# Optimization experiments

Hardware: AMD Instinct MI355X
Metric: run time of the kernel (lower is better)

## Reference

```python
import jax, jax.numpy as jnp
import numpy as np

EPS = 1e-6
N_HEADS, N_POINTS = 6, 4


def layer_norm(x, w, b):
    m = jnp.mean(x, -1, keepdims=True)
    v = jnp.mean((x - m) ** 2, -1, keepdims=True)
    return (x - m) * jax.lax.rsqrt(v + EPS) * w + b


def bilinear_sample(val, loc, Hl, Wl):
    # val: (B, nH, Hl*Wl, d); loc: (B, Lq, nH, P, 2) in [0,1]
    # matches F.grid_sample(mode='bilinear', padding='zeros', align_corners=False)
    B, nH, _, d = val.shape
    Lq, P = loc.shape[1], loc.shape[3]
    x = loc[..., 0] * Wl - 0.5
    y = loc[..., 1] * Hl - 0.5
    x0 = jnp.floor(x)
    y0 = jnp.floor(y)
    wx1 = x - x0
    wy1 = y - y0
    out = jnp.zeros((B, nH, Lq * P, d), val.dtype)
    corners = ((0, 0, (1 - wy1) * (1 - wx1)), (0, 1, (1 - wy1) * wx1),
               (1, 0, wy1 * (1 - wx1)), (1, 1, wy1 * wx1))
    for dy, dx, w in corners:
        xi = x0 + dx
        yi = y0 + dy
        valid = (xi >= 0) & (xi < Wl) & (yi >= 0) & (yi < Hl)
        xi_c = jnp.clip(xi, 0, Wl - 1).astype(jnp.int32)
        yi_c = jnp.clip(yi, 0, Hl - 1).astype(jnp.int32)
        idx = (yi_c * Wl + xi_c).transpose(0, 2, 1, 3).reshape(B, nH, Lq * P)
        g = jnp.take_along_axis(val, idx[..., None], axis=2)  # (B,nH,Lq*P,d)
        ww = jnp.where(valid, w, 0.0).transpose(0, 2, 1, 3).reshape(B, nH, Lq * P)
        out = out + g * ww[..., None]
    return out.reshape(B, nH, Lq, P, d).transpose(0, 2, 1, 3, 4)  # (B,Lq,nH,P,d)


def dwconv3x3(x, w, b):
    # x: (N, C, H, W); w: (C, 1, 3, 3) depthwise
    y = jax.lax.conv_general_dilated(x, w, (1, 1), 'SAME',
                                     feature_group_count=w.shape[0],
                                     dimension_numbers=('NCHW', 'OIHW', 'NCHW'))
    return y + b[None, :, None, None]


def setup_inputs() -> dict:
    key = jax.random.key(0)
    ks = jax.random.split(key, 16)
    B, H, W, C = 8, 32, 32, 768
    Lq = 3 * H * W
    Hf = Wf = 64
    hidden = int(C * 0.25)
    s = 0.02
    inp = {
        'query': jax.random.normal(ks[0], (B, Lq, C), jnp.float32),
        'reference_points': jax.random.uniform(ks[1], (B, Lq, 1, 2), jnp.float32),
        'feat': jax.random.normal(ks[2], (B, Hf * Wf, C), jnp.float32),
        'spatial_shapes': jnp.array([[Hf, Wf]], jnp.int32),
        'level_start_index': jnp.zeros((1,), jnp.int32),
        'H': H, 'W': W,
        'qn_w': jnp.ones((C,)), 'qn_b': jnp.zeros((C,)),
        'fn_w': jnp.ones((C,)), 'fn_b': jnp.zeros((C,)),
        'so_w': jax.random.normal(ks[3], (C, N_HEADS * N_POINTS * 2)) * s,
        'so_b': jax.random.normal(ks[4], (N_HEADS * N_POINTS * 2,)) * s,
        'aw_w': jax.random.normal(ks[5], (C, N_HEADS * N_POINTS)) * s,
        'aw_b': jnp.zeros((N_HEADS * N_POINTS,)),
        'vp_w': jax.random.normal(ks[6], (C, C)) * s,
        'vp_b': jnp.zeros((C,)),
        'op_w': jax.random.normal(ks[7], (C, C)) * s,
        'op_b': jnp.zeros((C,)),
        'ffn_w': jnp.ones((C,)), 'ffn_b': jnp.zeros((C,)),
        'fc1_w': jax.random.normal(ks[8], (C, hidden)) * s,
        'fc1_b': jnp.zeros((hidden,)),
        'dw_w': jax.random.normal(ks[9], (hidden, 1, 3, 3)) * s,
        'dw_b': jnp.zeros((hidden,)),
        'fc2_w': jax.random.normal(ks[10], (hidden, C)) * s,
        'fc2_b': jnp.zeros((C,)),
    }
    return inp


def reference(query, reference_points, feat, spatial_shapes, level_start_index, H, W,
              qn_w, qn_b, fn_w, fn_b, so_w, so_b, aw_w, aw_b, vp_w, vp_b, op_w, op_b,
              ffn_w, ffn_b, fc1_w, fc1_b, dw_w, dw_b, fc2_w, fc2_b):
    B, Lq, C = query.shape
    nH, nP = N_HEADS, N_POINTS
    d = C // nH
    ss = np.asarray(spatial_shapes)
    Hl, Wl = int(ss[0, 0]), int(ss[0, 1])

    # --- MSDeformAttn (single level) ---
    q = layer_norm(query, qn_w, qn_b)
    f = layer_norm(feat, fn_w, fn_b)
    value = (f @ vp_w + vp_b).reshape(B, Hl * Wl, nH, d).transpose(0, 2, 1, 3)  # (B,nH,Lin,d)
    offs = (q @ so_w + so_b).reshape(B, Lq, nH, 1, nP, 2)
    aw = jax.nn.softmax((q @ aw_w + aw_b).reshape(B, Lq, nH, nP), axis=-1)
    normalizer = jnp.array([Wl, Hl], query.dtype)
    loc = reference_points[:, :, None, :, None, :] + offs / normalizer  # (B,Lq,nH,1,nP,2)
    sampled = bilinear_sample(value, loc[:, :, :, 0], Hl, Wl)           # (B,Lq,nH,nP,d)
    attn = (sampled * aw[..., None]).sum(3).reshape(B, Lq, C) @ op_w + op_b
    query = query + attn

    # --- ConvFFN (3 equal HxW chunks through shared depthwise conv) ---
    x = layer_norm(query, ffn_w, ffn_b) @ fc1_w + fc1_b  # (B, 3*H*W, hid)
    n = Lq // 3
    hid = fc1_w.shape[1]
    xc = x.reshape(B, 3, n, hid).transpose(0, 1, 3, 2).reshape(B * 3, hid, H, W)
    xc = dwconv3x3(xc, dw_w, dw_b)
    x = xc.reshape(B, 3, hid, n).transpose(0, 1, 3, 2).reshape(B, Lq, hid)
    x = jax.nn.gelu(x, approximate=False)
    x = x @ fc2_w + fc2_b
    return query + x
```

## Files before the change

### kernel.cpp

```cpp
#include <hip/hip_runtime.h>
#include <hip/hip_bf16.h>
#include <math.h>

typedef __hip_bfloat16 bf16;
typedef short bf16x8 __attribute__((ext_vector_type(8)));
typedef float f32x4 __attribute__((ext_vector_type(4)));

#define NB 8
#define LQ 3072
#define CC 768
#define NHEADS 6
#define NPTS 4
#define DHEAD 128
#define HLVL 64
#define WLVL 64
#define LIN 4096
#define HID 192
#define BLTOT 24576
#define FROWS 32768

__global__ __launch_bounds__(256)
void ln_bf16_kernel(const float* __restrict__ x, const float* __restrict__ w,
                    const float* __restrict__ b, bf16* __restrict__ out)
{
    const int row = blockIdx.x;
    const int t = threadIdx.x;
    const float* xr = x + (size_t)row * CC;
    float v0 = xr[t], v1 = xr[t + 256], v2 = xr[t + 512];
    float s = v0 + v1 + v2;
    float ss = v0 * v0 + v1 * v1 + v2 * v2;
    #pragma unroll
    for (int o = 32; o > 0; o >>= 1) {
        s += __shfl_down(s, o);
        ss += __shfl_down(ss, o);
    }
    __shared__ float red[8];
    const int lane = t & 63, wv = t >> 6;
    if (lane == 0) { red[wv] = s; red[4 + wv] = ss; }
    __syncthreads();
    if (t == 0) {
        float S = red[0] + red[1] + red[2] + red[3];
        float SS = red[4] + red[5] + red[6] + red[7];
        float m = S * (1.f / CC);
        float var = SS * (1.f / CC) - m * m;
        red[0] = m; red[1] = rsqrtf(var + 1e-6f);
    }
    __syncthreads();
    const float m = red[0], rs = red[1];
    bf16* o = out + (size_t)row * CC;
    o[t]       = __float2bfloat16((v0 - m) * rs * w[t] + b[t]);
    o[t + 256] = __float2bfloat16((v1 - m) * rs * w[t + 256] + b[t + 256]);
    o[t + 512] = __float2bfloat16((v2 - m) * rs * w[t + 512] + b[t + 512]);
}

__global__ __launch_bounds__(256)
void wt_bf16_kernel(const float* __restrict__ src, bf16* __restrict__ dst, int K, int N)
{
    __shared__ float t[64][65];
    const int tn0 = blockIdx.x * 64, tk0 = blockIdx.y * 64;
    const int r = threadIdx.x >> 6, c = threadIdx.x & 63;
    #pragma unroll
    for (int i = 0; i < 16; ++i) {
        const int k = i * 4 + r;
        t[k][c] = src[(size_t)(tk0 + k) * N + tn0 + c];
    }
    __syncthreads();
    #pragma unroll
    for (int i = 0; i < 16; ++i) {
        const int n = i * 4 + r;
        dst[(size_t)(tn0 + n) * K + tk0 + c] = __float2bfloat16(t[c][n]);
    }
}

__global__ __launch_bounds__(256)
void build_dots_w(const float* __restrict__ so_w, const float* __restrict__ so_b,
                  const float* __restrict__ aw_w, const float* __restrict__ aw_b,
                  bf16* __restrict__ wt, float* __restrict__ db)
{
    int i = blockIdx.x * 256 + threadIdx.x;
    if (i < 128 * 768) {
        int n = i / 768, k = i - n * 768;
        float v = 0.f;
        if (n < 48) v = so_w[(size_t)k * 48 + n];
        else if (n < 72) v = aw_w[(size_t)k * 24 + (n - 48)];
        wt[i] = __float2bfloat16(v);
    }
    if (i < 128) {
        float bv = 0.f;
        if (i < 48) bv = so_b[i];
        else if (i < 72) bv = aw_b[i - 48];
        db[i] = bv;
    }
}

template<int N_>
__device__ __forceinline__ void wait_vmcnt()
{
    if constexpr (N_ == 0)      asm volatile("s_waitcnt vmcnt(0)" ::: "memory");
    else if constexpr (N_ == 4) asm volatile("s_waitcnt vmcnt(4)" ::: "memory");
    else if constexpr (N_ == 6) asm volatile("s_waitcnt vmcnt(6)" ::: "memory");
    else if constexpr (N_ == 8) asm volatile("s_waitcnt vmcnt(8)" ::: "memory");
    else static_assert(N_ == 0 || N_ == 4 || N_ == 6 || N_ == 8, "add a vmcnt case");
}

template<int BM, int BN, int WM, int WN, int MODE>
__global__ __launch_bounds__(256)
void gemm_kernel(const bf16* __restrict__ A, const bf16* __restrict__ Bt,
                 const float* __restrict__ bias, const float* __restrict__ res,
                 void* __restrict__ outv, int M, int N, int K)
{
    constexpr int WAVES_N = BN / WN;
    constexpr int FM = WM / 16, FN = WN / 16;
    constexpr int CWA = BM / 32;
    constexpr int CWB = BN / 32;
    constexpr int LPT = CWA + CWB;
    constexpr int ABYTES = BM * 256;
    constexpr int DBUF_BYTES = (BM + BN) * 256;
    constexpr int EPI_BYTES = BM * BN * 4;
    constexpr size_t SMEM_BYTES = DBUF_BYTES > EPI_BYTES ? DBUF_BYTES : EPI_BYTES;
    __shared__ __align__(16) char smem[SMEM_BYTES];
    bf16* sA = (bf16*)smem;
    bf16* sB = (bf16*)(smem + ABYTES);
    float* epi = (float*)smem;

    const int tid = threadIdx.x;
    const int lane = tid & 63;
    const int wave = tid >> 6;

    const int nwgx = gridDim.x;
    const int nwg = nwgx * gridDim.y;
    const int bid = blockIdx.y * nwgx + blockIdx.x;
    const int swz = (bid & 7) * (nwg >> 3) + (bid >> 3);
    const int m0 = (swz / nwgx) * BM;
    const int n0 = (swz % nwgx) * BN;

    const int wm = (wave / WAVES_N) * WM;
    const int wn = (wave % WAVES_N) * WN;

    const int srow = lane >> 3;
    const int scol = ((lane & 7) ^ srow) * 8;

#define STAGE(tt, half)                                                                            \
    { const int k0_ = (tt) * 64;                                                                   \
      _Pragma("unroll")                                                                            \
      for (int i_ = 0; i_ < CWA; ++i_) {                                                           \
        const int c_ = i_ * 4 + wave;                                                              \
        __builtin_amdgcn_global_load_lds(                                                          \
          (const __attribute__((address_space(1))) void*)(A + (size_t)(m0 + c_ * 8 + srow) * K + k0_ + scol), \
          (__attribute__((address_space(3))) void*)(sA + (half) * (BM * 64) + c_ * 512), 16, 0, 0); } \
      _Pragma("unroll")                                                                            \
      for (int i_ = 0; i_ < CWB; ++i_) {                                                           \
        const int c_ = i_ * 4 + wave;                                                              \
        __builtin_amdgcn_global_load_lds(                                                          \
          (const __attribute__((address_space(1))) void*)(Bt + (size_t)(n0 + c_ * 8 + srow) * K + k0_ + scol), \
          (__attribute__((address_space(3))) void*)(sB + (half) * (BN * 64) + c_ * 512), 16, 0, 0); } }

    f32x4 acc[FM][FN] = {};
    const int nt = K >> 6;

    STAGE(0, 0);
    STAGE(1, 1);

    for (int t = 0; t < nt; ++t) {
        const int half = t & 1;
        if (t + 1 < nt) wait_vmcnt<LPT>();
        else            wait_vmcnt<0>();
        __builtin_amdgcn_s_barrier();
        const bf16* cA = sA + half * (BM * 64);
        const bf16* cB = sB + half * (BN * 64);
        #pragma unroll
        for (int kki = 0; kki < 2; ++kki) {
            const int kslot = kki * 4 + (lane >> 4);
            bf16x8 aF[FM], bF[FN];
            #pragma unroll
            for (int i = 0; i < FM; ++i) {
                const int row = wm + i * 16 + (lane & 15);
                aF[i] = *(const bf16x8*)(&cA[row * 64 + ((kslot ^ (row & 7)) * 8)]);
            }
            #pragma unroll
            for (int j = 0; j < FN; ++j) {
                const int row = wn + j * 16 + (lane & 15);
                bF[j] = *(const bf16x8*)(&cB[row * 64 + ((kslot ^ (row & 7)) * 8)]);
            }
            #pragma unroll
            for (int i = 0; i < FM; ++i) {
                #pragma unroll
                for (int j = 0; j < FN; ++j)
                    acc[i][j] = __builtin_amdgcn_mfma_f32_16x16x32_bf16(aF[i], bF[j], acc[i][j], 0, 0, 0);
            }
        }
        asm volatile("s_waitcnt lgkmcnt(0)" ::: "memory");
        __builtin_amdgcn_s_barrier();
        if (t + 2 < nt) STAGE(t + 2, half);
    }
#undef STAGE

    #pragma unroll
    for (int j = 0; j < FN; ++j) {
        const int colL = wn + j * 16 + (lane & 15);
        const float bj = bias[n0 + colL];
        #pragma unroll
        for (int i = 0; i < FM; ++i) {
            #pragma unroll
            for (int r = 0; r < 4; ++r) {
                const int rowL = wm + i * 16 + ((lane >> 4) << 2) + r;
                const int addr = rowL * BN + ((((colL >> 2) ^ (rowL & 7)) << 2) | (colL & 3));
                epi[addr] = acc[i][j][r] + bj;
            }
        }
    }
    __syncthreads();

    if constexpr (MODE == 0) {
        constexpr int GPR = BN / 8;
        constexpr int GPT = (BM * BN / 8) / 256;
        #pragma unroll
        for (int k = 0; k < GPT; ++k) {
            const int f = k * 256 + tid;
            const int rr = f / GPR, cc = (f % GPR) * 8;
            const int g0 = ((cc >> 2) ^ (rr & 7)) << 2;
            const int g1 = (((cc >> 2) + 1) ^ (rr & 7)) << 2;
            float4 v0 = *(const float4*)&epi[rr * BN + g0];
            float4 v1 = *(const float4*)&epi[rr * BN + g1];
            bf16 tmp[8];
            tmp[0] = __float2bfloat16(v0.x); tmp[1] = __float2bfloat16(v0.y);
            tmp[2] = __float2bfloat16(v0.z); tmp[3] = __float2bfloat16(v0.w);
            tmp[4] = __float2bfloat16(v1.x); tmp[5] = __float2bfloat16(v1.y);
            tmp[6] = __float2bfloat16(v1.z); tmp[7] = __float2bfloat16(v1.w);
            *(bf16x8*)((bf16*)outv + (size_t)(m0 + rr) * N + n0 + cc) = *(bf16x8*)tmp;
        }
    } else {
        constexpr int QPR = BN / 4;
        constexpr int QPT = (BM * BN / 4) / 256;
        #pragma unroll
        for (int k = 0; k < QPT; ++k) {
            const int f = k * 256 + tid;
            const int rr = f / QPR, cc = (f % QPR) * 4;
            const int gs = ((cc >> 2) ^ (rr & 7)) << 2;
            float4 v = *(const float4*)&epi[rr * BN + gs];
            const size_t gidx = (size_t)(m0 + rr) * N + n0 + cc;
            if constexpr (MODE == 1) {
                float4 q = *(const float4*)&res[gidx];
                v.x += q.x; v.y += q.y; v.z += q.z; v.w += q.w;
            }
            *(float4*)&((float*)outv)[gidx] = v;
        }
    }
}

__global__ __launch_bounds__(256)
void locsoftmax_kernel(const float* __restrict__ dots, const float* __restrict__ refp,
                       float4* __restrict__ params)
{
    int i = blockIdx.x * 256 + threadIdx.x;
    if (i >= BLTOT * NHEADS) return;
    int bl = i / NHEADS, h = i - bl * NHEADS;
    const float* d = dots + (size_t)bl * 128;
    float rx = refp[(size_t)bl * 2], ry = refp[(size_t)bl * 2 + 1];
    float l0 = d[48 + h * 4 + 0], l1 = d[48 + h * 4 + 1];
    float l2 = d[48 + h * 4 + 2], l3 = d[48 + h * 4 + 3];
    float mx = fmaxf(fmaxf(l0, l1), fmaxf(l2, l3));
    float e0 = expf(l0 - mx), e1 = expf(l1 - mx), e2 = expf(l2 - mx), e3 = expf(l3 - mx);
    float inv = 1.f / (e0 + e1 + e2 + e3);
    float ee[4] = {e0, e1, e2, e3};
    #pragma unroll
    for (int p = 0; p < 4; ++p) {
        float ox = d[h * 8 + p * 2], oy = d[h * 8 + p * 2 + 1];
        params[(size_t)i * 4 + p] =
            make_float4(rx + ox * (1.f / WLVL), ry + oy * (1.f / HLVL), ee[p] * inv, 0.f);
    }
}

__global__ __launch_bounds__(256)
void sampler_kernel(const bf16* __restrict__ value, const float4* __restrict__ params,
                    bf16* __restrict__ attn_in)
{
    const int tid = threadIdx.x;
    const int g = blockIdx.x * 16 + (tid >> 4);
    const int lane16 = tid & 15;
    const int bl = g / NHEADS;
    const int h = g - bl * NHEADS;
    const int b = bl / LQ;
    const bf16* vh = value + (size_t)b * LIN * CC + h * DHEAD + lane16 * 8;

    int offs[16];
    float wgt[16];
    #pragma unroll
    for (int p = 0; p < NPTS; ++p) {
        float4 pr = params[(size_t)g * 4 + p];
        float x = pr.x * (float)WLVL - 0.5f;
        float y = pr.y * (float)HLVL - 0.5f;
        float x0f = floorf(x), y0f = floorf(y);
        float wx1 = x - x0f, wy1 = y - y0f;
        float wx0 = 1.f - wx1, wy0 = 1.f - wy1;
        int x0 = (int)x0f, y0 = (int)y0f;
        #pragma unroll
        for (int dy = 0; dy < 2; ++dy) {
            const int yi = y0 + dy;
            const int yc = min(max(yi, 0), HLVL - 1);
            const float wy = (dy ? wy1 : wy0) * ((yi >= 0 && yi < HLVL) ? pr.z : 0.f);
            #pragma unroll
            for (int dx = 0; dx < 2; ++dx) {
                const int xi = x0 + dx;
                const int xc = min(max(xi, 0), WLVL - 1);
                const int idx = p * 4 + dy * 2 + dx;
                offs[idx] = (yc * WLVL + xc) * CC;
                wgt[idx] = wy * (dx ? wx1 : wx0) * ((xi >= 0 && xi < WLVL) ? 1.f : 0.f);
            }
        }
    }
    bf16x8 v[16];
    #pragma unroll
    for (int i = 0; i < 16; ++i) v[i] = *(const bf16x8*)(vh + offs[i]);
    float acc[8] = {};
    #pragma unroll
    for (int i = 0; i < 16; ++i) {
        #pragma unroll
        for (int j = 0; j < 8; ++j)
            acc[j] += wgt[i] * __uint_as_float(((unsigned)(unsigned short)v[i][j]) << 16);
    }
    bf16 tmp[8];
    #pragma unroll
    for (int j = 0; j < 8; ++j) tmp[j] = __float2bfloat16(acc[j]);
    *(bf16x8*)(attn_in + (size_t)bl * CC + h * DHEAD + lane16 * 8) = *(bf16x8*)tmp;
}

__global__ void dwconv_gelu_kernel(const float* __restrict__ z, const float* __restrict__ dw_w,
                                   const float* __restrict__ dw_b, bf16* __restrict__ g)
{
    const int m = blockIdx.x;
    const int c = threadIdx.x;
    const int pix = m & 1023;
    const int h = pix >> 5, w = pix & 31;
    float acc = dw_b[c];
    #pragma unroll
    for (int dy = -1; dy <= 1; ++dy) {
        int hh2 = h + dy;
        if (hh2 < 0 || hh2 >= 32) continue;
        #pragma unroll
        for (int dx = -1; dx <= 1; ++dx) {
            int ww2 = w + dx;
            if (ww2 < 0 || ww2 >= 32) continue;
            acc += z[(size_t)(m + dy * 32 + dx) * HID + c] * dw_w[c * 9 + (dy + 1) * 3 + (dx + 1)];
        }
    }
    float ge = acc * 0.5f * (1.f + erff(acc * 0.70710678118f));
    g[(size_t)m * HID + c] = __float2bfloat16(ge);
}

extern "C" void kernel_launch(void* const* d_in, const int* in_sizes, int n_in,
                              void* d_out, int out_size, void* d_ws, size_t ws_size,
                              hipStream_t stream)
{
    const float* query = (const float*)d_in[0];
    const float* refp  = (const float*)d_in[1];
    const float* feat  = (const float*)d_in[2];
    const float* qn_w = (const float*)d_in[7];
    const float* qn_b = (const float*)d_in[8];
    const float* fn_w = (const float*)d_in[9];
    const float* fn_b = (const float*)d_in[10];
    const float* so_w = (const float*)d_in[11];
    const float* so_b = (const float*)d_in[12];
    const float* aw_w = (const float*)d_in[13];
    const float* aw_b = (const float*)d_in[14];
    const float* vp_w = (const float*)d_in[15];
    const float* vp_b = (const float*)d_in[16];
    const float* op_w = (const float*)d_in[17];
    const float* op_b = (const float*)d_in[18];
    const float* ffn_w = (const float*)d_in[19];
    const float* ffn_b = (const float*)d_in[20];
    const float* fc1_w = (const float*)d_in[21];
    const float* fc1_b = (const float*)d_in[22];
    const float* dw_w = (const float*)d_in[23];
    const float* dw_b = (const float*)d_in[24];
    const float* fc2_w = (const float*)d_in[25];
    const float* fc2_b = (const float*)d_in[26];
    float* out = (float*)d_out;

    if (ws_size < (size_t)125829632) return;
    char* ws = (char*)d_ws;
    bf16* vp_wt   = (bf16*)(ws + 0);
    bf16* op_wt   = (bf16*)(ws + 1179648);
    bf16* fc1_wt  = (bf16*)(ws + 2359296);
    bf16* fc2_wt  = (bf16*)(ws + 2654208);
    bf16* dots_wt = (bf16*)(ws + 2949120);
    float* dots_b = (float*)(ws + 3145728);
    float4* params = (float4*)(ws + 3146240);
    float* dots_out = (float*)(ws + 12583424);
    char* regA = ws + 25166336;
    char* regB = ws + 75497984;
    bf16* f_ln    = (bf16*)regA;
    bf16* attn_in = (bf16*)regA;
    float* z      = (float*)regA;
    bf16* q_ln  = (bf16*)regB;
    bf16* value = (bf16*)regB;
    bf16* y     = (bf16*)regB;
    bf16* g     = (bf16*)regB;

    wt_bf16_kernel<<<dim3(12, 12), 256, 0, stream>>>(vp_w, vp_wt, 768, 768);
    wt_bf16_kernel<<<dim3(12, 12), 256, 0, stream>>>(op_w, op_wt, 768, 768);
    wt_bf16_kernel<<<dim3(3, 12), 256, 0, stream>>>(fc1_w, fc1_wt, 768, 192);
    wt_bf16_kernel<<<dim3(12, 3), 256, 0, stream>>>(fc2_w, fc2_wt, 192, 768);
    build_dots_w<<<384, 256, 0, stream>>>(so_w, so_b, aw_w, aw_b, dots_wt, dots_b);

    ln_bf16_kernel<<<BLTOT, 256, 0, stream>>>(query, qn_w, qn_b, q_ln);
    gemm_kernel<64, 128, 32, 64, 2><<<dim3(1, BLTOT / 64), 256, 0, stream>>>(
        q_ln, dots_wt, dots_b, nullptr, dots_out, BLTOT, 128, 768);
    locsoftmax_kernel<<<(BLTOT * NHEADS + 255) / 256, 256, 0, stream>>>(dots_out, refp, params);
    ln_bf16_kernel<<<FROWS, 256, 0, stream>>>(feat, fn_w, fn_b, f_ln);
    gemm_kernel<128, 128, 64, 64, 0><<<dim3(6, FROWS / 128), 256, 0, stream>>>(
        f_ln, vp_wt, vp_b, nullptr, value, FROWS, 768, 768);
    sampler_kernel<<<(BLTOT * NHEADS) / 16, 256, 0, stream>>>(value, params, attn_in);
    gemm_kernel<64, 128, 32, 64, 1><<<dim3(6, BLTOT / 64), 256, 0, stream>>>(
        attn_in, op_wt, op_b, query, out, BLTOT, 768, 768);

    ln_bf16_kernel<<<BLTOT, 256, 0, stream>>>(out, ffn_w, ffn_b, y);
    gemm_kernel<64, 64, 16, 64, 2><<<dim3(3, BLTOT / 64), 256, 0, stream>>>(
        y, fc1_wt, fc1_b, nullptr, z, BLTOT, HID, 768);
    dwconv_gelu_kernel<<<BLTOT, HID, 0, stream>>>(z, dw_w, dw_b, g);
    gemm_kernel<64, 128, 32, 64, 1><<<dim3(6, BLTOT / 64), 256, 0, stream>>>(
        g, fc2_wt, fc2_b, out, out, BLTOT, 768, HID);
}
```

Measured before the change: 347.6 us.

## Store intermediate residual and fc1 output in bf16, prefetch residual, vectorize LN/dwconv

The attention output-projection GEMM now writes the residual sum as bf16 instead of fp32, and the FFN LayerNorm reads that bf16 tensor with a wave-per-row vectorized kernel. fc1 output is stored in bf16, and the depthwise conv + GELU kernel processes four channels per thread with vector loads. The final GEMM adds a bf16 residual that is prefetched into registers before the main loop, and the dots GEMM uses a smaller tile to launch more blocks. This cuts memory traffic across several stages but rounds the residual stream to bf16, which reduces accuracy of the final output.

```diff
diff --git a/kernel.cpp b/kernel.cpp
--- a/kernel.cpp
+++ b/kernel.cpp
@@ -4,6 +4,7 @@
 
 typedef __hip_bfloat16 bf16;
 typedef short bf16x8 __attribute__((ext_vector_type(8)));
+typedef short bf16x4 __attribute__((ext_vector_type(4)));
 typedef float f32x4 __attribute__((ext_vector_type(4)));
 
 #define NB 8
@@ -19,6 +20,9 @@
 #define BLTOT 24576
 #define FROWS 32768
 
+__device__ __forceinline__ float bf2f(short u)
+{ return __uint_as_float(((unsigned)(unsigned short)u) << 16); }
+
 __global__ __launch_bounds__(256)
 void ln_bf16_kernel(const float* __restrict__ x, const float* __restrict__ w,
                     const float* __restrict__ b, bf16* __restrict__ out)
@@ -54,6 +58,48 @@
 }
 
 __global__ __launch_bounds__(256)
+void ln_bf16in_kernel(const bf16* __restrict__ x, const float* __restrict__ w,
+                      const float* __restrict__ b, bf16* __restrict__ out)
+{
+    const int row = blockIdx.x * 4 + (threadIdx.x >> 6);
+    const int lane = threadIdx.x & 63;
+    const bf16* xr = x + (size_t)row * CC;
+    bf16x8 v8 = *(const bf16x8*)(xr + lane * 8);
+    bf16x4 v4 = *(const bf16x4*)(xr + 512 + lane * 4);
+    float v[12];
+    #pragma unroll
+    for (int j = 0; j < 8; ++j) v[j] = bf2f(v8[j]);
+    #pragma unroll
+    for (int j = 0; j < 4; ++j) v[8 + j] = bf2f(v4[j]);
+    float s = 0.f, ss = 0.f;
+    #pragma unroll
+    for (int j = 0; j < 12; ++j) { s += v[j]; ss += v[j] * v[j]; }
+    #pragma unroll
+    for (int o = 32; o > 0; o >>= 1) {
+        s += __shfl_down(s, o);
+        ss += __shfl_down(ss, o);
+    }
+    s = __shfl(s, 0); ss = __shfl(ss, 0);
+    const float m = s * (1.f / CC);
+    const float rs = rsqrtf(ss * (1.f / CC) - m * m + 1e-6f);
+    float wv[12], bv[12];
+    *(float4*)&wv[0] = *(const float4*)&w[lane * 8];
+    *(float4*)&wv[4] = *(const float4*)&w[lane * 8 + 4];
+    *(float4*)&wv[8] = *(const float4*)&w[512 + lane * 4];
+    *(float4*)&bv[0] = *(const float4*)&b[lane * 8];
+    *(float4*)&bv[4] = *(const float4*)&b[lane * 8 + 4];
+    *(float4*)&bv[8] = *(const float4*)&b[512 + lane * 4];
+    bf16 o8[8], o4[4];
+    #pragma unroll
+    for (int j = 0; j < 8; ++j) o8[j] = __float2bfloat16((v[j] - m) * rs * wv[j] + bv[j]);
+    #pragma unroll
+    for (int j = 0; j < 4; ++j) o4[j] = __float2bfloat16((v[8 + j] - m) * rs * wv[8 + j] + bv[8 + j]);
+    bf16* orow = out + (size_t)row * CC;
+    *(bf16x8*)(orow + lane * 8) = *(bf16x8*)o8;
+    *(bf16x4*)(orow + 512 + lane * 4) = *(bf16x4*)o4;
+}
+
+__global__ __launch_bounds__(256)
 void wt_bf16_kernel(const float* __restrict__ src, bf16* __restrict__ dst, int K, int N)
 {
     __shared__ float t[64][65];
@@ -98,15 +144,16 @@
 {
     if constexpr (N_ == 0)      asm volatile("s_waitcnt vmcnt(0)" ::: "memory");
     else if constexpr (N_ == 4) asm volatile("s_waitcnt vmcnt(4)" ::: "memory");
+    else if constexpr (N_ == 5) asm volatile("s_waitcnt vmcnt(5)" ::: "memory");
     else if constexpr (N_ == 6) asm volatile("s_waitcnt vmcnt(6)" ::: "memory");
     else if constexpr (N_ == 8) asm volatile("s_waitcnt vmcnt(8)" ::: "memory");
-    else static_assert(N_ == 0 || N_ == 4 || N_ == 6 || N_ == 8, "add a vmcnt case");
+    else static_assert(N_ == 0, "add a vmcnt case");
 }
 
 template<int BM, int BN, int WM, int WN, int MODE>
 __global__ __launch_bounds__(256)
 void gemm_kernel(const bf16* __restrict__ A, const bf16* __restrict__ Bt,
-                 const float* __restrict__ bias, const float* __restrict__ res,
+                 const float* __restrict__ bias, const void* __restrict__ resv,
                  void* __restrict__ outv, int M, int N, int K)
 {
     constexpr int WAVES_N = BN / WN;
@@ -139,6 +186,33 @@
 
     const int srow = lane >> 3;
     const int scol = ((lane & 7) ^ srow) * 8;
+
+    constexpr int GPR8 = BN / 8;
+    constexpr int GPT8 = (BM * BN / 8) / 256;
+    constexpr int QPR4 = BN / 4;
+    constexpr int QPT4 = (BM * BN / 4) / 256;
+    float4 pr0[GPT8], pr1[GPT8];
+    bf16x4 prb[QPT4];
+    if constexpr (MODE == 3) {
+        const float* resf = (const float*)resv;
+        #pragma unroll
+        for (int k = 0; k < GPT8; ++k) {
+            const int f = k * 256 + tid;
+            const int rr = f / GPR8, cc = (f % GPR8) * 8;
+            const size_t gidx = (size_t)(m0 + rr) * N + n0 + cc;
+            pr0[k] = *(const float4*)&resf[gidx];
+            pr1[k] = *(const float4*)&resf[gidx + 4];
+        }
+    }
+    if constexpr (MODE == 4) {
+        const bf16* resb = (const bf16*)resv;
+        #pragma unroll
+        for (int k = 0; k < QPT4; ++k) {
+            const int f = k * 256 + tid;
+            const int rr = f / QPR4, cc = (f % QPR4) * 4;
+            prb[k] = *(const bf16x4*)&resb[(size_t)(m0 + rr) * N + n0 + cc];
+        }
+    }
 
 #define STAGE(tt, half)                                                                            \
     { const int k0_ = (tt) * 64;                                                                   \
@@ -211,17 +285,19 @@
     }
     __syncthreads();
 
-    if constexpr (MODE == 0) {
-        constexpr int GPR = BN / 8;
-        constexpr int GPT = (BM * BN / 8) / 256;
-        #pragma unroll
-        for (int k = 0; k < GPT; ++k) {
+    if constexpr (MODE == 0 || MODE == 3) {
+        #pragma unroll
+        for (int k = 0; k < GPT8; ++k) {
             const int f = k * 256 + tid;
-            const int rr = f / GPR, cc = (f % GPR) * 8;
+            const int rr = f / GPR8, cc = (f % GPR8) * 8;
             const int g0 = ((cc >> 2) ^ (rr & 7)) << 2;
             const int g1 = (((cc >> 2) + 1) ^ (rr & 7)) << 2;
             float4 v0 = *(const float4*)&epi[rr * BN + g0];
             float4 v1 = *(const float4*)&epi[rr * BN + g1];
+            if constexpr (MODE == 3) {
+                v0.x += pr0[k].x; v0.y += pr0[k].y; v0.z += pr0[k].z; v0.w += pr0[k].w;
+                v1.x += pr1[k].x; v1.y += pr1[k].y; v1.z += pr1[k].z; v1.w += pr1[k].w;
+            }
             bf16 tmp[8];
             tmp[0] = __float2bfloat16(v0.x); tmp[1] = __float2bfloat16(v0.y);
             tmp[2] = __float2bfloat16(v0.z); tmp[3] = __float2bfloat16(v0.w);
@@ -230,20 +306,17 @@
             *(bf16x8*)((bf16*)outv + (size_t)(m0 + rr) * N + n0 + cc) = *(bf16x8*)tmp;
         }
     } else {
-        constexpr int QPR = BN / 4;
-        constexpr int QPT = (BM * BN / 4) / 256;
-        #pragma unroll
-        for (int k = 0; k < QPT; ++k) {
+        #pragma unroll
+        for (int k = 0; k < QPT4; ++k) {
             const int f = k * 256 + tid;
-            const int rr = f / QPR, cc = (f % QPR) * 4;
+            const int rr = f / QPR4, cc = (f % QPR4) * 4;
             const int gs = ((cc >> 2) ^ (rr & 7)) << 2;
             float4 v = *(const float4*)&epi[rr * BN + gs];
-            const size_t gidx = (size_t)(m0 + rr) * N + n0 + cc;
-            if constexpr (MODE == 1) {
-                float4 q = *(const float4*)&res[gidx];
-                v.x += q.x; v.y += q.y; v.z += q.z; v.w += q.w;
-            }
-            *(float4*)&((float*)outv)[gidx] = v;
+            if constexpr (MODE == 4) {
+                v.x += bf2f(prb[k][0]); v.y += bf2f(prb[k][1]);
+                v.z += bf2f(prb[k][2]); v.w += bf2f(prb[k][3]);
+            }
+            *(float4*)&((float*)outv)[(size_t)(m0 + rr) * N + n0 + cc] = v;
         }
     }
 }
@@ -317,7 +390,7 @@
     for (int i = 0; i < 16; ++i) {
         #pragma unroll
         for (int j = 0; j < 8; ++j)
-            acc[j] += wgt[i] * __uint_as_float(((unsigned)(unsigned short)v[i][j]) << 16);
+            acc[j] += wgt[i] * bf2f(v[i][j]);
     }
     bf16 tmp[8];
     #pragma unroll
@@ -325,14 +398,19 @@
     *(bf16x8*)(attn_in + (size_t)bl * CC + h * DHEAD + lane16 * 8) = *(bf16x8*)tmp;
 }
 
-__global__ void dwconv_gelu_kernel(const float* __restrict__ z, const float* __restrict__ dw_w,
-                                   const float* __restrict__ dw_b, bf16* __restrict__ g)
-{
-    const int m = blockIdx.x;
-    const int c = threadIdx.x;
+__global__ __launch_bounds__(192)
+void dwconv_gelu_kernel(const bf16* __restrict__ z, const float* __restrict__ dw_w,
+                        const float* __restrict__ dw_b, bf16* __restrict__ g)
+{
+    const int tp = threadIdx.x / 48;
+    const int tc = threadIdx.x % 48;
+    const int m = blockIdx.x * 4 + tp;
+    const int c = tc * 4;
     const int pix = m & 1023;
     const int h = pix >> 5, w = pix & 31;
-    float acc = dw_b[c];
+    float acc[4];
+    #pragma unroll
+    for (int j = 0; j < 4; ++j) acc[j] = dw_b[c + j];
     #pragma unroll
     for (int dy = -1; dy <= 1; ++dy) {
         int hh2 = h + dy;
@@ -341,11 +419,19 @@
         for (int dx = -1; dx <= 1; ++dx) {
             int ww2 = w + dx;
             if (ww2 < 0 || ww2 >= 32) continue;
-            acc += z[(size_t)(m + dy * 32 + dx) * HID + c] * dw_w[c * 9 + (dy + 1) * 3 + (dx + 1)];
-        }
-    }
-    float ge = acc * 0.5f * (1.f + erff(acc * 0.70710678118f));
-    g[(size_t)m * HID + c] = __float2bfloat16(ge);
+            bf16x4 vv = *(const bf16x4*)&z[(size_t)(m + dy * 32 + dx) * HID + c];
+            #pragma unroll
+            for (int j = 0; j < 4; ++j)
+                acc[j] += bf2f(vv[j]) * dw_w[(c + j) * 9 + (dy + 1) * 3 + (dx + 1)];
+        }
+    }
+    bf16 tmp[4];
+    #pragma unroll
+    for (int j = 0; j < 4; ++j) {
+        float ge = acc[j] * 0.5f * (1.f + erff(acc[j] * 0.70710678118f));
+        tmp[j] = __float2bfloat16(ge);
+    }
+    *(bf16x4*)&g[(size_t)m * HID + c] = *(bf16x4*)tmp;
 }
 
 extern "C" void kernel_launch(void* const* d_in, const int* in_sizes, int n_in,
@@ -385,17 +471,20 @@
     bf16* fc2_wt  = (bf16*)(ws + 2654208);
     bf16* dots_wt = (bf16*)(ws + 2949120);
     float* dots_b = (float*)(ws + 3145728);
-    float4* params = (float4*)(ws + 3146240);
-    float* dots_out = (float*)(ws + 12583424);
+    char* paramsR = ws + 3146240;
+    char* dotsR   = ws + 12583424;
     char* regA = ws + 25166336;
     char* regB = ws + 75497984;
+    float4* params = (float4*)paramsR;
+    bf16* g        = (bf16*)paramsR;
+    float* dots_out = (float*)dotsR;
+    bf16* z         = (bf16*)dotsR;
     bf16* f_ln    = (bf16*)regA;
     bf16* attn_in = (bf16*)regA;
-    float* z      = (float*)regA;
+    bf16* y       = (bf16*)regA;
     bf16* q_ln  = (bf16*)regB;
     bf16* value = (bf16*)regB;
-    bf16* y     = (bf16*)regB;
-    bf16* g     = (bf16*)regB;
+    bf16* s_bf  = (bf16*)regB;
 
     wt_bf16_kernel<<<dim3(12, 12), 256, 0, stream>>>(vp_w, vp_wt, 768, 768);
     wt_bf16_kernel<<<dim3(12, 12), 256, 0, stream>>>(op_w, op_wt, 768, 768);
@@ -404,20 +493,20 @@
     build_dots_w<<<384, 256, 0, stream>>>(so_w, so_b, aw_w, aw_b, dots_wt, dots_b);
 
     ln_bf16_kernel<<<BLTOT, 256, 0, stream>>>(query, qn_w, qn_b, q_ln);
-    gemm_kernel<64, 128, 32, 64, 2><<<dim3(1, BLTOT / 64), 256, 0, stream>>>(
+    gemm_kernel<32, 128, 16, 64, 2><<<dim3(1, BLTOT / 32), 256, 0, stream>>>(
         q_ln, dots_wt, dots_b, nullptr, dots_out, BLTOT, 128, 768);
     locsoftmax_kernel<<<(BLTOT * NHEADS + 255) / 256, 256, 0, stream>>>(dots_out, refp, params);
     ln_bf16_kernel<<<FROWS, 256, 0, stream>>>(feat, fn_w, fn_b, f_ln);
     gemm_kernel<128, 128, 64, 64, 0><<<dim3(6, FROWS / 128), 256, 0, stream>>>(
         f_ln, vp_wt, vp_b, nullptr, value, FROWS, 768, 768);
     sampler_kernel<<<(BLTOT * NHEADS) / 16, 256, 0, stream>>>(value, params, attn_in);
-    gemm_kernel<64, 128, 32, 64, 1><<<dim3(6, BLTOT / 64), 256, 0, stream>>>(
-        attn_in, op_wt, op_b, query, out, BLTOT, 768, 768);
-
-    ln_bf16_kernel<<<BLTOT, 256, 0, stream>>>(out, ffn_w, ffn_b, y);
-    gemm_kernel<64, 64, 16, 64, 2><<<dim3(3, BLTOT / 64), 256, 0, stream>>>(
+    gemm_kernel<64, 128, 32, 64, 3><<<dim3(6, BLTOT / 64), 256, 0, stream>>>(
+        attn_in, op_wt, op_b, query, s_bf, BLTOT, 768, 768);
+
+    ln_bf16in_kernel<<<BLTOT / 4, 256, 0, stream>>>(s_bf, ffn_w, ffn_b, y);
+    gemm_kernel<64, 64, 16, 64, 0><<<dim3(3, BLTOT / 64), 256, 0, stream>>>(
         y, fc1_wt, fc1_b, nullptr, z, BLTOT, HID, 768);
-    dwconv_gelu_kernel<<<BLTOT, HID, 0, stream>>>(z, dw_w, dw_b, g);
-    gemm_kernel<64, 128, 32, 64, 1><<<dim3(6, BLTOT / 64), 256, 0, stream>>>(
-        g, fc2_wt, fc2_b, out, out, BLTOT, 768, HID);
-}
+    dwconv_gelu_kernel<<<BLTOT / 4, 192, 0, stream>>>(z, dw_w, dw_b, g);
+    gemm_kernel<64, 128, 32, 64, 4><<<dim3(6, BLTOT / 64), 256, 0, stream>>>(
+        g, fc2_wt, fc2_b, s_bf, out, BLTOT, 768, HID);
+}
```

New measurement: 342.9 us. About the same (-1.3%).
